# Optimization experiments

Hardware: AMD Instinct MI355X
Metric: run time of the kernel (lower is better)

## Reference

```python
import jax, jax.numpy as jnp
import numpy as np

NHEAD = 8
DC = 32
IN_CHS = 2 * NHEAD  # cross_coverage and self_coverage both True
EPS = 1e-5  # BatchNorm1d default eps


def conv2d(x, w, pad):
    return jax.lax.conv_general_dilated(
        x, w, window_strides=(1, 1), padding=[(pad, pad), (pad, pad)],
        dimension_numbers=('NCHW', 'OIHW', 'NCHW'))


def setup_inputs() -> dict:
    key = jax.random.key(0)
    ks = jax.random.split(key, 10)
    b, t, H, W = 8, 256, 16, 32
    l = H * W
    prev_attn = jax.random.uniform(ks[0], (b * NHEAD, t, l), dtype=jnp.float32)
    curr_attn = jax.random.uniform(ks[1], (b * NHEAD, t, l), dtype=jnp.float32)
    key_padding_mask = jax.random.uniform(ks[2], (b, l)) < 0.25  # True = padded
    conv_w = jax.random.normal(ks[3], (DC, IN_CHS, 5, 5), jnp.float32) * 0.05
    conv_b = jnp.zeros((DC,), jnp.float32)
    proj_w = jax.random.normal(ks[4], (NHEAD, DC, 1, 1), jnp.float32) * 0.05
    g_w1 = jax.random.normal(ks[5], (IN_CHS // 2, IN_CHS, 3, 3), jnp.float32) * 0.05
    g_b1 = jnp.zeros((IN_CHS // 2,), jnp.float32)
    g_w2 = jax.random.normal(ks[6], (IN_CHS, IN_CHS // 2, 1, 1), jnp.float32) * 0.05
    g_b2 = jnp.zeros((IN_CHS,), jnp.float32)
    bn_gamma = jnp.ones((NHEAD,), jnp.float32)
    bn_beta = jnp.zeros((NHEAD,), jnp.float32)
    return dict(prev_attn=prev_attn, key_padding_mask=key_padding_mask, h=H,
                curr_attn=curr_attn, tgt_vocab=113,
                conv_w=conv_w, conv_b=conv_b, proj_w=proj_w,
                g_w1=g_w1, g_b1=g_b1, g_w2=g_w2, g_b2=g_b2,
                bn_gamma=bn_gamma, bn_beta=bn_beta)


def reference(prev_attn, key_padding_mask, h, curr_attn, tgt_vocab,
              conv_w, conv_b, proj_w, g_w1, g_b1, g_w2, g_b2, bn_gamma, bn_beta):
    n = NHEAD
    b = prev_attn.shape[0] // n
    t = curr_attn.shape[1]
    l = key_padding_mask.shape[1]
    w = l // h

    prev = prev_attn.reshape(b, n, t, l)
    curr = curr_attn.reshape(b, n, t, l)
    attns = jnp.concatenate([prev, curr], axis=1)  # [b, 2n, t, l]
    c = attns.shape[1]

    # gating network on per-step attention images: [(b t), c, h, w]
    attns_bt = attns.transpose(0, 2, 1, 3).reshape(b * t, c, h, w)
    g = jax.nn.relu(conv2d(attns_bt, g_w1, 1) + g_b1[None, :, None, None])
    g = g.mean(axis=(2, 3))  # AdaptiveAvgPool2d((1,1)) -> [(b t), c//2]
    g = jax.nn.sigmoid(jnp.einsum('bi,oi->bo', g, g_w2[:, :, 0, 0]) + g_b2)
    gate = g.reshape(b, t, c).transpose(0, 2, 1)[..., None]  # [b, c, t, 1]

    gated = attns * gate
    cum = jnp.cumsum(gated, axis=2) - gated  # exclusive cumulative coverage
    cum2d = cum.transpose(0, 2, 1, 3).reshape(b * t, c, h, w)

    mask = jnp.broadcast_to(key_padding_mask.reshape(b, 1, 1, h, w),
                            (b, t, 1, h, w)).reshape(b * t, 1, h, w)

    cov = jax.nn.relu(conv2d(cum2d, conv_w, 2) + conv_b[None, :, None, None])
    cov = jnp.where(mask, 0.0, cov)
    cov = jnp.einsum('bdhw,nd->bnhw', cov, proj_w[:, :, 0, 0])  # 1x1 proj, no bias

    # MaskBatchNorm2d: BN statistics over non-masked positions only
    nm = (~mask).astype(cov.dtype)  # [(b t), 1, h, w]
    cnt = nm.sum()
    mean = (cov * nm).sum(axis=(0, 2, 3), keepdims=True) / cnt  # per-channel
    var = (jnp.square(cov - mean) * nm).sum(axis=(0, 2, 3), keepdims=True) / cnt
    xn = (cov - mean) * jax.lax.rsqrt(var + EPS) * bn_gamma[None, :, None, None] \
        + bn_beta[None, :, None, None]
    cov = jnp.where(mask, cov, xn)  # masked positions keep pre-BN values (zeros)

    out = cov.reshape(b, t, n, l).transpose(0, 2, 1, 3).reshape(b * n, t, l)
    return out
```

## Files before the change

kernel.cpp:

```cpp
#include <hip/hip_runtime.h>
#include <hip/hip_bf16.h>

#define BB   8
#define TT   256
#define NH   8
#define CC   16
#define HH   16
#define WW   32
#define LL   512
#define DCH  32
#define GC   8

#define PSC  1928
#define PSG  1736

typedef __attribute__((ext_vector_type(8))) short s8b;
typedef __attribute__((ext_vector_type(4))) float f32x4;

__device__ __forceinline__ ushort f2bfu(float v) {
  __hip_bfloat16 h = __float2bfloat16(v);
  ushort s;
  __builtin_memcpy(&s, &h, 2);
  return s;
}

__global__ __launch_bounds__(256) void k_gen(const float* __restrict__ cw,
                                             const float* __restrict__ pw,
                                             const float* __restrict__ gw1,
                                             ushort* __restrict__ bfrag,
                                             ushort* __restrict__ pwf,
                                             ushort* __restrict__ bfragG,
                                             float* __restrict__ sums) {
  int idx = blockIdx.x * 256 + threadIdx.x;
  if (idx < 17) sums[idx] = 0.f;
  if (idx < 13312) {
    int j = idx & 7, lane = (idx >> 3) & 63, nt = (idx >> 9) & 1, s = idx >> 10;
    int quad = lane >> 4, col = lane & 15;
    int k = s * 32 + quad * 8 + j;
    int n = nt * 16 + col;
    float v = (k < 400) ? cw[(n * CC + (k & 15)) * 25 + (k >> 4)] : 0.f;
    bfrag[idx] = f2bfu(v);
  } else if (idx < 13824) {
    int i2 = idx - 13312;
    int j = i2 & 7, lane = i2 >> 3;
    int quad = lane >> 4, col = lane & 15;
    float v = (col < NH) ? pw[col * DCH + quad * 8 + j] : 0.f;
    pwf[i2] = f2bfu(v);
  } else if (idx < 16384) {
    int i3 = idx - 13824;
    int j = i3 & 7, lane = (i3 >> 3) & 63, s = i3 >> 9;
    int quad = lane >> 4, col = lane & 15;
    int k = s * 32 + quad * 8 + j;
    float v = 0.f;
    if (k < 144 && col < GC) v = gw1[(col * CC + (k & 15)) * 9 + (k >> 4)];
    bfragG[i3] = f2bfu(v);
  }
}

__global__ __launch_bounds__(256) void k_gate(
    const float* __restrict__ prev, const float* __restrict__ curr,
    const ushort* __restrict__ bfragG, const float* __restrict__ gb1,
    const float* __restrict__ gw2, const float* __restrict__ gb2,
    float* __restrict__ gate2) {
  __shared__ __align__(16) ushort img[8 * PSG];
  __shared__ float redg[64];
  __shared__ float pooled[16];

  int tid = threadIdx.x;
  int lane = tid & 63, w = tid >> 6;
  int bt = blockIdx.x;
  int b = bt >> 8, t = bt & 255;
  int quad = lane >> 4, col = lane & 15;
  int qh = quad >> 1, icb = (quad & 1) * 8;

  for (int i = tid; i < PSG; i += 256) ((uint4*)img)[i] = (uint4){0, 0, 0, 0};
  __syncthreads();

#pragma unroll
  for (int it = 0; it < 4; ++it) {
#pragma unroll
    for (int e = 0; e < 2; ++e) {
      int W = ((it * 4 + w) * 2 + e) * 64 + lane;
      int cp = W >> 8, pp = W & 255;
      int l0 = pp * 2;
      const float* src = (cp < 4) ? prev : curr;
      int chb = (cp & 3) * 2;
      const float* p0 = src + ((size_t)(b * NH + chb) * TT + t) * LL + l0;
      float2 fa = *(const float2*)p0;
      float2 fb = *(const float2*)(p0 + TT * LL);
      unsigned lo = (unsigned)f2bfu(fa.x) | ((unsigned)f2bfu(fb.x) << 16);
      unsigned hi = (unsigned)f2bfu(fa.y) | ((unsigned)f2bfu(fb.y) << 16);
      int r = l0 >> 5, x = l0 & 31;
      int slot = (r + 1) * 48 + 8 + x;
      *(uint2*)&img[cp * PSG + slot * 2] = (uint2){lo, hi};
    }
  }
  __syncthreads();

  f32x4 acc[8];
#pragma unroll
  for (int mi = 0; mi < 8; ++mi) acc[mi] = (f32x4){0.f, 0.f, 0.f, 0.f};
  int mtbase = w * 8;
  int ab[8];
#pragma unroll
  for (int mi = 0; mi < 8; ++mi) {
    int mt = mtbase + mi;
    int py = mt >> 1, px = ((mt & 1) << 4) + col;
    ab[mi] = (icb >> 1) * PSG + (py * 48 + 7 + px) * 2;
  }
  const int offE[5] = {0, 2, 49, 96, 98};
  const int offO[5] = {1, 48, 50, 97, 98};
  const s8b* bG = (const s8b*)bfragG;
#pragma unroll
  for (int s = 0; s < 5; ++s) {
    s8b bf = bG[s * 64 + lane];
    int off2 = (qh ? offO[s] : offE[s]) * 2;
#pragma unroll
    for (int mi = 0; mi < 8; ++mi) {
      union { unsigned u[4]; s8b v; } A;
      int a0 = ab[mi] + off2;
#pragma unroll
      for (int p = 0; p < 4; ++p) A.u[p] = *(const unsigned*)&img[a0 + p * PSG];
      acc[mi] = __builtin_amdgcn_mfma_f32_16x16x32_bf16(A.v, bf, acc[mi], 0, 0, 0);
    }
  }

  float gb1c = (col < GC) ? gb1[col] : 0.f;
  float s = 0.f;
#pragma unroll
  for (int mi = 0; mi < 8; ++mi)
#pragma unroll
    for (int r = 0; r < 4; ++r) s += fmaxf(acc[mi][r] + gb1c, 0.f);
  s += __shfl_down(s, 16, 64);
  s += __shfl_down(s, 32, 64);
  if (lane < 16) redg[w * 16 + lane] = s;
  __syncthreads();
  if (tid < 16)
    pooled[tid] = (redg[tid] + redg[16 + tid] + redg[32 + tid] + redg[48 + tid]) *
                  (1.0f / (float)LL);
  __syncthreads();
  if (tid < 16) {
    float z = gb2[tid];
#pragma unroll
    for (int i = 0; i < GC; ++i) z = fmaf(pooled[i], gw2[tid * GC + i], z);
    gate2[(b * CC + tid) * TT + t] = 1.f / (1.f + __expf(-z));
  }
}

__global__ __launch_bounds__(256) void k_cum(const float* __restrict__ prev,
                                             const float* __restrict__ curr,
                                             const float* __restrict__ gate2,
                                             ushort* __restrict__ cum) {
  int idx = blockIdx.x * 256 + threadIdx.x;
  int l = idx & 511;
  int c = (idx >> 9) & 15;
  int b = idx >> 13;
  const float* src = (c < NH) ? prev : curr;
  const float* a = src + (size_t)(b * NH + (c & 7)) * TT * LL + l;
  const float* g = gate2 + (b * CC + c) * TT;
  ushort* o = cum + (size_t)(b * CC + c) * TT * LL + l;
  float run = 0.f;
#pragma unroll 8
  for (int t = 0; t < TT; ++t) {
    float av = a[(size_t)t * LL];
    float gv = g[t];
    o[(size_t)t * LL] = f2bfu(run);
    run = fmaf(av, gv, run);
  }
}

__global__ __launch_bounds__(256, 2) void k_cov(
    const ushort* __restrict__ cum, const ushort* __restrict__ bfrag,
    const ushort* __restrict__ pwf, const float* __restrict__ cb,
    const int* __restrict__ mask, float* __restrict__ out,
    float* __restrict__ sums) {
  __shared__ __align__(16) ushort img[8 * PSC];
  __shared__ __align__(16) ushort scr[4 * 640];
  __shared__ float redp[128];
  __shared__ float redc[4];

  int tid = threadIdx.x;
  int lane = tid & 63, w = tid >> 6;
  int bt = blockIdx.x;
  int b = bt >> 8, t = bt & 255;
  int quad = lane >> 4, col = lane & 15;
  int qh = quad >> 1, icb = (quad & 1) * 8;

  for (int i = tid; i < PSC; i += 256) ((uint4*)img)[i] = (uint4){0, 0, 0, 0};
  __syncthreads();

#pragma unroll
  for (int it = 0; it < 4; ++it) {
#pragma unroll
    for (int e = 0; e < 2; ++e) {
      int W = ((it * 4 + w) * 2 + e) * 64 + lane;
      int cp = W >> 8, pp = W & 255;
      int l0 = pp * 2;
      const ushort* p0 = cum + ((size_t)(b * CC + cp * 2) * TT + t) * LL + l0;
      unsigned a = *(const unsigned*)p0;
      unsigned bb2 = *(const unsigned*)(p0 + TT * LL);
      unsigned lo = (a & 0xFFFFu) | (bb2 << 16);
      unsigned hi = (a >> 16) | (bb2 & 0xFFFF0000u);
      int r = l0 >> 5, x = l0 & 31;
      int slot = (r + 2) * 48 + 8 + x;
      *(uint2*)&img[cp * PSC + slot * 2] = (uint2){lo, hi};
    }
  }
  __syncthreads();

  f32x4 acc[8][2];
#pragma unroll
  for (int mi = 0; mi < 8; ++mi) {
    acc[mi][0] = (f32x4){0.f, 0.f, 0.f, 0.f};
    acc[mi][1] = (f32x4){0.f, 0.f, 0.f, 0.f};
  }
  int mtbase = w * 8;
  int ab[8];
#pragma unroll
  for (int mi = 0; mi < 8; ++mi) {
    int mt = mtbase + mi;
    int py = mt >> 1, px = ((mt & 1) << 4) + col;
    ab[mi] = (icb >> 1) * PSC + (py * 48 + 6 + px) * 2;
  }
  const int offE[13] = {0, 2, 4, 49, 51, 96, 98, 100, 145, 147, 192, 194, 196};
  const int offO[13] = {1, 3, 48, 50, 52, 97, 99, 144, 146, 148, 193, 195, 196};
  const s8b* bfr = (const s8b*)bfrag;
#pragma unroll
  for (int s = 0; s < 13; ++s) {
    s8b bf0 = bfr[(s * 2) * 64 + lane];
    s8b bf1 = bfr[(s * 2 + 1) * 64 + lane];
    int off2 = (qh ? offO[s] : offE[s]) * 2;
#pragma unroll
    for (int mi = 0; mi < 8; ++mi) {
      union { unsigned u[4]; s8b v; } A;
      int a0 = ab[mi] + off2;
#pragma unroll
      for (int p = 0; p < 4; ++p) A.u[p] = *(const unsigned*)&img[a0 + p * PSC];
      acc[mi][0] = __builtin_amdgcn_mfma_f32_16x16x32_bf16(A.v, bf0, acc[mi][0], 0, 0, 0);
      acc[mi][1] = __builtin_amdgcn_mfma_f32_16x16x32_bf16(A.v, bf1, acc[mi][1], 0, 0, 0);
    }
  }

  int wb = w * 640;
  float cb0 = cb[col], cb1 = cb[col + 16];
  s8b pf = ((const s8b*)pwf)[lane];
  float psum = 0.f, psq = 0.f, pcnt = 0.f;
  float* outbase = out + ((size_t)(b * NH + col) * TT + t) * LL;
  const int* mrow = mask + b * LL;
#pragma unroll
  for (int mi = 0; mi < 8; ++mi) {
    int mt = mtbase + mi;
    ushort w0[4], w1[4];
#pragma unroll
    for (int r = 0; r < 4; ++r) {
      w0[r] = f2bfu(fmaxf(acc[mi][0][r] + cb0, 0.f));
      w1[r] = f2bfu(fmaxf(acc[mi][1][r] + cb1, 0.f));
    }
    uint2 pk0, pk1;
    __builtin_memcpy(&pk0, w0, 8);
    __builtin_memcpy(&pk1, w1, 8);
    *(uint2*)&scr[wb + col * 20 + quad * 4] = pk0;
    *(uint2*)&scr[wb + (col + 16) * 20 + quad * 4] = pk1;
    ushort u[8];
#pragma unroll
    for (int e = 0; e < 8; ++e) u[e] = scr[wb + (quad * 8 + e) * 20 + col];
    s8b a2;
    __builtin_memcpy(&a2, u, 16);
    f32x4 zero = {0.f, 0.f, 0.f, 0.f};
    f32x4 d2 = __builtin_amdgcn_mfma_f32_16x16x32_bf16(a2, pf, zero, 0, 0, 0);
    int4 m4 = *(const int4*)(mrow + mt * 16 + quad * 4);
    float k0 = m4.x ? 0.f : 1.f;
    float k1 = m4.y ? 0.f : 1.f;
    float k2 = m4.z ? 0.f : 1.f;
    float k3 = m4.w ? 0.f : 1.f;
    if (col < NH) {
      float* op = outbase + mt * 16 + quad * 4;
      float v0 = d2[0] * k0; op[0] = v0; psum += v0; psq += v0 * v0;
      float v1 = d2[1] * k1; op[1] = v1; psum += v1; psq += v1 * v1;
      float v2 = d2[2] * k2; op[2] = v2; psum += v2; psq += v2 * v2;
      float v3 = d2[3] * k3; op[3] = v3; psum += v3; psq += v3 * v3;
    }
    if (col == 0) pcnt += k0 + k1 + k2 + k3;
  }

  psum += __shfl_down(psum, 16, 64); psum += __shfl_down(psum, 32, 64);
  psq  += __shfl_down(psq, 16, 64);  psq  += __shfl_down(psq, 32, 64);
  pcnt += __shfl_down(pcnt, 16, 64); pcnt += __shfl_down(pcnt, 32, 64);
  if (lane < 16) {
    redp[(w * 16 + lane) * 2] = psum;
    redp[(w * 16 + lane) * 2 + 1] = psq;
    if (lane == 0) redc[w] = pcnt;
  }
  __syncthreads();
  if (tid < 17) {
    float v;
    if (tid < 8) {
      v = redp[tid * 2] + redp[(16 + tid) * 2] + redp[(32 + tid) * 2] + redp[(48 + tid) * 2];
    } else if (tid < 16) {
      int nh = tid - 8;
      v = redp[nh * 2 + 1] + redp[(16 + nh) * 2 + 1] + redp[(32 + nh) * 2 + 1] + redp[(48 + nh) * 2 + 1];
    } else {
      v = redc[0] + redc[1] + redc[2] + redc[3];
    }
    atomicAdd(&sums[tid], v);
  }
}

__global__ __launch_bounds__(256) void k_bn(
    float* __restrict__ out, const float* __restrict__ sums,
    const int* __restrict__ mask, const float* __restrict__ gamma,
    const float* __restrict__ beta) {
  __shared__ float sc[NH], sh[NH];
  int tid = threadIdx.x;
  if (tid < NH) {
    float cnt = sums[16];
    float mean = sums[tid] / cnt;
    float var = sums[NH + tid] / cnt - mean * mean;
    float inv = rsqrtf(var + 1e-5f) * gamma[tid];
    sc[tid] = inv;
    sh[tid] = fmaf(-mean, inv, beta[tid]);
  }
  __syncthreads();
  size_t e = ((size_t)blockIdx.x * 256 + tid) * 4;
  int l = (int)(e & (LL - 1));
  int bn = (int)(e >> 17);
  int n = bn & 7, b = bn >> 3;
  const int4 mv = *(const int4*)(mask + b * LL + l);
  float4 v = *(float4*)(out + e);
  float s = sc[n], h = sh[n];
  v.x = mv.x ? v.x : fmaf(v.x, s, h);
  v.y = mv.y ? v.y : fmaf(v.y, s, h);
  v.z = mv.z ? v.z : fmaf(v.z, s, h);
  v.w = mv.w ? v.w : fmaf(v.w, s, h);
  *(float4*)(out + e) = v;
}

extern "C" void kernel_launch(void* const* d_in, const int* in_sizes, int n_in,
                              void* d_out, int out_size, void* d_ws, size_t ws_size,
                              hipStream_t stream) {
  const float* prev   = (const float*)d_in[0];
  const int*   mask   = (const int*)d_in[1];
  const float* curr   = (const float*)d_in[3];
  const float* conv_w = (const float*)d_in[5];
  const float* conv_b = (const float*)d_in[6];
  const float* proj_w = (const float*)d_in[7];
  const float* g_w1   = (const float*)d_in[8];
  const float* g_b1   = (const float*)d_in[9];
  const float* g_w2   = (const float*)d_in[10];
  const float* g_b2   = (const float*)d_in[11];
  const float* bn_g   = (const float*)d_in[12];
  const float* bn_b   = (const float*)d_in[13];
  float* out = (float*)d_out;

  char* ws = (char*)d_ws;
  ushort* bfrag  = (ushort*)(ws);
  ushort* pwf    = (ushort*)(ws + 26624);
  ushort* bfragG = (ushort*)(ws + 27648);
  float*  sums   = (float*)(ws + 32768);
  float*  gate2  = (float*)(ws + 36864);
  ushort* cum    = (ushort*)(ws + 36864 + 131072);

  k_gen<<<64, 256, 0, stream>>>(conv_w, proj_w, g_w1, bfrag, pwf, bfragG, sums);
  k_gate<<<BB * TT, 256, 0, stream>>>(prev, curr, bfragG, g_b1, g_w2, g_b2, gate2);
  k_cum<<<(BB * CC * LL) / 256, 256, 0, stream>>>(prev, curr, gate2, cum);
  k_cov<<<BB * TT, 256, 0, stream>>>(cum, bfrag, pwf, conv_b, mask, out, sums);
  k_bn<<<(BB * NH * TT * LL) / (256 * 4), 256, 0, stream>>>(out, sums, mask, bn_g, bn_b);
}
```

Baseline: 204.4 us.

## Split cumulative-sum scan over time chunks and raise occupancy bounds

The exclusive cumsum kernel previously ran one thread per (b,c,l) scanning all 256 steps, which gives only 256 blocks and a long serial dependency chain. It now splits time into four 64-step chunks per block. Each chunk first computes its partial sum, combines the preceding chunks' sums through shared memory, then rescans to write the output. This costs reading the input twice in exchange for four times the parallelism. Launch bounds for k_gate and k_cov are also raised to 4 blocks per SM, which may force register spills.

```diff
diff --git a/kernel.cpp b/kernel.cpp
--- a/kernel.cpp
+++ b/kernel.cpp
@@ -57,7 +57,7 @@
   }
 }
 
-__global__ __launch_bounds__(256) void k_gate(
+__global__ __launch_bounds__(256, 4) void k_gate(
     const float* __restrict__ prev, const float* __restrict__ curr,
     const ushort* __restrict__ bfragG, const float* __restrict__ gb1,
     const float* __restrict__ gw2, const float* __restrict__ gb2,
@@ -151,25 +151,36 @@
                                              const float* __restrict__ curr,
                                              const float* __restrict__ gate2,
                                              ushort* __restrict__ cum) {
-  int idx = blockIdx.x * 256 + threadIdx.x;
-  int l = idx & 511;
-  int c = (idx >> 9) & 15;
-  int b = idx >> 13;
+  __shared__ float cs[256];
+  int bid = blockIdx.x;
+  int lg = bid & 7;
+  int c = (bid >> 3) & 15;
+  int b = bid >> 7;
+  int tid = threadIdx.x;
+  int li = tid & 63, tc = tid >> 6;
+
   const float* src = (c < NH) ? prev : curr;
-  const float* a = src + (size_t)(b * NH + (c & 7)) * TT * LL + l;
-  const float* g = gate2 + (b * CC + c) * TT;
-  ushort* o = cum + (size_t)(b * CC + c) * TT * LL + l;
+  const float* a = src + ((size_t)(b * NH + (c & 7)) * TT + tc * 64) * LL + lg * 64 + li;
+  const float* g = gate2 + (b * CC + c) * TT + tc * 64;
+
+  float s = 0.f;
+#pragma unroll 8
+  for (int j = 0; j < 64; ++j) s = fmaf(a[(size_t)j * LL], g[j], s);
+  cs[tc * 64 + li] = s;
+  __syncthreads();
+
   float run = 0.f;
+  for (int u = 0; u < tc; ++u) run += cs[u * 64 + li];
+
+  ushort* o = cum + ((size_t)(b * CC + c) * TT + tc * 64) * LL + lg * 64 + li;
 #pragma unroll 8
-  for (int t = 0; t < TT; ++t) {
-    float av = a[(size_t)t * LL];
-    float gv = g[t];
-    o[(size_t)t * LL] = f2bfu(run);
-    run = fmaf(av, gv, run);
-  }
-}
-
-__global__ __launch_bounds__(256, 2) void k_cov(
+  for (int j = 0; j < 64; ++j) {
+    o[(size_t)j * LL] = f2bfu(run);
+    run = fmaf(a[(size_t)j * LL], g[j], run);
+  }
+}
+
+__global__ __launch_bounds__(256, 4) void k_cov(
     const ushort* __restrict__ cum, const ushort* __restrict__ bfrag,
     const ushort* __restrict__ pwf, const float* __restrict__ cb,
     const int* __restrict__ mask, float* __restrict__ out,
@@ -362,7 +373,7 @@
 
   k_gen<<<64, 256, 0, stream>>>(conv_w, proj_w, g_w1, bfrag, pwf, bfragG, sums);
   k_gate<<<BB * TT, 256, 0, stream>>>(prev, curr, bfragG, g_b1, g_w2, g_b2, gate2);
-  k_cum<<<(BB * CC * LL) / 256, 256, 0, stream>>>(prev, curr, gate2, cum);
+  k_cum<<<BB * CC * 8, 256, 0, stream>>>(prev, curr, gate2, cum);
   k_cov<<<BB * TT, 256, 0, stream>>>(cum, bfrag, pwf, conv_b, mask, out, sums);
   k_bn<<<(BB * NH * TT * LL) / (256 * 4), 256, 0, stream>>>(out, sums, mask, bn_g, bn_b);
 }
```

Measured after the change: 208.6 us. 1.02x slower.
